# Optimization experiments

Measured on AMD Instinct MI355X. Metric: run time of the kernel, lower is better.

## Reference

```python
import jax, jax.numpy as jnp
import numpy as np

B = 8
H1c = W1c = 56
H2c = W2c = 112
C1 = 512
C2 = 256
NH = 8
WS = 7
POOL = 2
EPS = 1e-5


def setup_inputs() -> dict:
    key = jax.random.key(0)
    ks = jax.random.split(key, 8)
    x = jax.random.normal(ks[0], (B, H1c * W1c, C1), dtype=jnp.float32)
    y = jax.random.normal(ks[1], (B, H2c * W2c, C2), dtype=jnp.float32)
    Wq = jax.random.normal(ks[2], (C1, C1), dtype=jnp.float32) * 0.02
    Wkv = jax.random.normal(ks[3], (2 * C1, C2), dtype=jnp.float32) * 0.02
    Wproj = jax.random.normal(ks[4], (C1, C1), dtype=jnp.float32) * 0.02
    bproj = jnp.zeros((C1,), dtype=jnp.float32)
    # 1x1 conv: fan_out = out_channels -> std = sqrt(2/C2)
    Wsr = jax.random.normal(ks[5], (C2, C2), dtype=jnp.float32) * np.sqrt(2.0 / C2).astype(np.float32)
    bsr = jnp.zeros((C2,), dtype=jnp.float32)
    gn = jnp.ones((C2,), dtype=jnp.float32)
    bn = jnp.zeros((C2,), dtype=jnp.float32)
    return {"x": x, "y": y, "Wq": Wq, "Wkv": Wkv, "Wproj": Wproj,
            "bproj": bproj, "Wsr": Wsr, "bsr": bsr, "gn": gn, "bn": bn,
            "H1": H1c, "W1": W1c, "H2": H2c, "W2": W2c}


def _window_partition(t, ws):
    # t: (B, nh, H, W, C) -> (B*nh, num_windows, ws*ws, C)
    Bt, n, H, W, C = t.shape
    ht, wt = H // ws, W // ws
    t = t.reshape(Bt, n, ht, ws, wt, ws, C).transpose(0, 1, 2, 4, 3, 5, 6)
    return t.reshape(Bt * n, ht * wt, ws * ws, C)


def reference(x, y, Wq, Wkv, Wproj, bproj, Wsr, bsr, gn, bn, H1, W1, H2, W2):
    B1, N1, c1 = x.shape
    B2, N2, c2 = y.shape
    nh, ws = NH, WS
    hd = c1 // nh
    scale = hd ** (-0.5)

    # q projection -> (B, nh, H1, W1, hd)
    q = (x @ Wq.T).reshape(B1, H1, W1, nh, hd).transpose(0, 3, 1, 2, 4)

    # KV preprocessing: avgpool -> 1x1 conv -> layernorm -> gelu
    y2 = y.transpose(0, 2, 1).reshape(B2, c2, H2, W2)
    Hp, Wp = H2 // POOL, W2 // POOL
    y2 = y2.reshape(B2, c2, Hp, POOL, Wp, POOL).mean(axis=(3, 5))
    y2 = jnp.einsum('bchw,oc->bohw', y2, Wsr) + bsr[None, :, None, None]
    y2 = y2.reshape(B2, c2, Hp * Wp).transpose(0, 2, 1)  # (B, Np, C2)
    mu = y2.mean(-1, keepdims=True)
    var = y2.var(-1, keepdims=True)
    y2 = (y2 - mu) / jnp.sqrt(var + EPS) * gn + bn
    y2 = jax.nn.gelu(y2, approximate=False)

    kv = (y2 @ Wkv.T).reshape(B2, Hp * Wp, 2, nh, hd)
    k = kv[:, :, 0].transpose(0, 2, 1, 3).reshape(B2, nh, Hp, Wp, hd)
    v = kv[:, :, 1].transpose(0, 2, 1, 3).reshape(B2, nh, Hp, Wp, hd)

    qw = _window_partition(q, ws)   # (B*nh, nw, ws^2, hd)
    kw = _window_partition(k, ws)
    vw = _window_partition(v, ws)

    attn = jax.nn.softmax(jnp.einsum('bnqd,bnkd->bnqk', qw, kw) * scale, axis=-1)
    out = jnp.einsum('bnqk,bnkd->bnqd', attn, vw)  # (B*nh, nw, ws^2, hd)

    # window reverse -> (B, N1, C1)
    ht, wt = H1 // ws, W1 // ws
    out = out.reshape(B1, nh, ht, wt, ws, ws, hd).transpose(0, 1, 2, 4, 3, 5, 6)
    out = out.reshape(B1, nh, H1 * W1, hd).transpose(0, 2, 1, 3).reshape(B1, H1 * W1, c1)
    return out @ Wproj.T + bproj
```

## Files before the change

### kernel.cpp

```cpp
#include <hip/hip_runtime.h>
#include <hip/hip_bf16.h>

typedef __attribute__((ext_vector_type(8))) short short8;
typedef __attribute__((ext_vector_type(4))) float f32x4;
typedef __attribute__((ext_vector_type(4))) unsigned short ushort4v;

#define DI __device__ __forceinline__

DI unsigned short f2bf(float f) {
  union { float f; unsigned int u; } a; a.f = f;
  unsigned int u = a.u;
  return (unsigned short)((u + 0x7FFFu + ((u >> 16) & 1u)) >> 16);
}

#define BARRIER() do { asm volatile("" ::: "memory"); __builtin_amdgcn_s_barrier(); asm volatile("" ::: "memory"); } while (0)
#define GLOAD16(src, dst) __builtin_amdgcn_global_load_lds( \
    (const __attribute__((address_space(1))) void*)(src), \
    (__attribute__((address_space(3))) void*)(dst), 16, 0, 0)


__global__ __launch_bounds__(256)
void cvt_pool(const float* __restrict__ y, unsigned short* __restrict__ pooled,
              const float* __restrict__ Wq, const float* __restrict__ Wkv,
              const float* __restrict__ Wproj, const float* __restrict__ Wsr,
              unsigned short* __restrict__ Wq_b, unsigned short* __restrict__ Wkv_b,
              unsigned short* __restrict__ Wproj_b, unsigned short* __restrict__ Wsr_b) {
  int bid = blockIdx.x;
  if (bid < 6272) {
    int t = bid * 256 + threadIdx.x;
    int cv = (t & 63) * 4;
    int bp = t >> 6;
    int b = bp / 3136, p = bp % 3136;
    int hp = p / 56, wp = p % 56;
    const float* src = y + (((size_t)b * 12544) + hp * 224 + wp * 2) * 256 + cv;
    float4 a0 = *(const float4*)(src);
    float4 a1 = *(const float4*)(src + 256);
    float4 a2 = *(const float4*)(src + 28672);
    float4 a3 = *(const float4*)(src + 28672 + 256);
    float4 av;
    av.x = (a0.x + a1.x + a2.x + a3.x) * 0.25f;
    av.y = (a0.y + a1.y + a2.y + a3.y) * 0.25f;
    av.z = (a0.z + a1.z + a2.z + a3.z) * 0.25f;
    av.w = (a0.w + a1.w + a2.w + a3.w) * 0.25f;
    ushort4v o = { f2bf(av.x), f2bf(av.y), f2bf(av.z), f2bf(av.w) };
    *(ushort4v*)&pooled[(size_t)bp * 256 + cv] = o;
  } else {
    long i = (long)(bid - 6272) * 1024 + threadIdx.x * 4;
    const float* src; unsigned short* dst; long off;
    if (i < 262144L)      { src = Wq;    dst = Wq_b;    off = i; }
    else if (i < 524288L) { src = Wkv;   dst = Wkv_b;   off = i - 262144L; }
    else if (i < 786432L) { src = Wproj; dst = Wproj_b; off = i - 524288L; }
    else                  { src = Wsr;   dst = Wsr_b;   off = i - 786432L; }
    float4 v = *(const float4*)&src[off];
    ushort4v o = { f2bf(v.x), f2bf(v.y), f2bf(v.z), f2bf(v.w) };
    *(ushort4v*)&dst[off] = o;
  }
}

__global__ __launch_bounds__(256)
void sr_gemm(const unsigned short* __restrict__ Ap, const unsigned short* __restrict__ Wsr_b,
             const float* __restrict__ bsr, const float* __restrict__ gn,
             const float* __restrict__ bn, unsigned short* __restrict__ out) {
  __shared__ unsigned short sA[64 * 64];
  __shared__ unsigned short sB[256 * 64];
  __shared__ float red[64 * 8];

  const int tid = threadIdx.x;
  const int wv = tid >> 6;
  const int lane = tid & 63;
  const int lr = lane & 15;
  const int lg = lane >> 4;
  const int lr4 = lg * 4;
  const int m0 = blockIdx.x * 64;
  const int sr8 = lane >> 3;
  const int sl8 = lane & 7;

  f32x4 acc[4][4];
#pragma unroll
  for (int i = 0; i < 4; ++i)
#pragma unroll
    for (int j = 0; j < 4; ++j) acc[i][j] = (f32x4){0.f, 0.f, 0.f, 0.f};

  for (int kt = 0; kt < 256; kt += 64) {
#pragma unroll
    for (int c = 0; c < 2; ++c) {
      int row = wv * 16 + c * 8 + sr8;
      GLOAD16(Ap + (size_t)(m0 + row) * 256 + kt + ((sl8 ^ (row & 7)) * 8),
              &sA[(wv * 16 + c * 8) * 64]);
    }
#pragma unroll
    for (int c = 0; c < 8; ++c) {
      int row = wv * 64 + c * 8 + sr8;
      GLOAD16(Wsr_b + (size_t)row * 256 + kt + ((sl8 ^ (row & 7)) * 8),
              &sB[(wv * 64 + c * 8) * 64]);
    }
    __syncthreads();
#pragma unroll
    for (int ks = 0; ks < 2; ++ks) {
      short8 af[4], bfr[4];
#pragma unroll
      for (int i = 0; i < 4; ++i)
        af[i] = *(const short8*)&sA[(i * 16 + lr) * 64 + (((ks * 4 + lg) ^ (lr & 7)) * 8)];
#pragma unroll
      for (int j = 0; j < 4; ++j)
        bfr[j] = *(const short8*)&sB[(wv * 64 + j * 16 + lr) * 64 + (((ks * 4 + lg) ^ (lr & 7)) * 8)];
#pragma unroll
      for (int i = 0; i < 4; ++i)
#pragma unroll
        for (int j = 0; j < 4; ++j)
          acc[i][j] = __builtin_amdgcn_mfma_f32_16x16x32_bf16(af[i], bfr[j], acc[i][j], 0, 0, 0);
    }
    __syncthreads();
  }

  float bsv[4], gnv[4], bnv[4];
#pragma unroll
  for (int j = 0; j < 4; ++j) {
    int col = wv * 64 + j * 16 + lr;
    bsv[j] = bsr[col]; gnv[j] = gn[col]; bnv[j] = bn[col];
  }
  float s_[4][4], q_[4][4];
#pragma unroll
  for (int i = 0; i < 4; ++i)
#pragma unroll
    for (int r = 0; r < 4; ++r) {
      float s = 0.f, q = 0.f;
#pragma unroll
      for (int j = 0; j < 4; ++j) {
        float v = acc[i][j][r] + bsv[j];
        acc[i][j][r] = v;
        s += v; q += v * v;
      }
      s_[i][r] = s; q_[i][r] = q;
    }
#pragma unroll
  for (int m = 1; m <= 8; m <<= 1)
#pragma unroll
    for (int i = 0; i < 4; ++i)
#pragma unroll
      for (int r = 0; r < 4; ++r) {
        s_[i][r] += __shfl_xor(s_[i][r], m);
        q_[i][r] += __shfl_xor(q_[i][r], m);
      }
  if (lr == 0) {
#pragma unroll
    for (int i = 0; i < 4; ++i)
#pragma unroll
      for (int r = 0; r < 4; ++r) {
        int row = i * 16 + lr4 + r;
        red[row * 8 + wv * 2 + 0] = s_[i][r];
        red[row * 8 + wv * 2 + 1] = q_[i][r];
      }
  }
  __syncthreads();
#pragma unroll
  for (int i = 0; i < 4; ++i) {
#pragma unroll
    for (int r = 0; r < 4; ++r) {
      int row = i * 16 + lr4 + r;
      float sum = red[row * 8 + 0] + red[row * 8 + 2] + red[row * 8 + 4] + red[row * 8 + 6];
      float sq  = red[row * 8 + 1] + red[row * 8 + 3] + red[row * 8 + 5] + red[row * 8 + 7];
      float mean = sum * (1.f / 256.f);
      float var = sq * (1.f / 256.f) - mean * mean;
      float rstd = rsqrtf(var + 1e-5f);
#pragma unroll
      for (int j = 0; j < 4; ++j) {
        float t = (acc[i][j][r] - mean) * rstd * gnv[j] + bnv[j];
        t = 0.5f * t * (1.f + erff(t * 0.70710678118654752f));
        out[(size_t)(m0 + row) * 256 + wv * 64 + j * 16 + lr] = f2bf(t);
      }
    }
  }
}

DI void epi_q(int gm, int gc, float v, unsigned short* outp) {
  const int b = gm / 3136, pos = gm % 3136;
  const int h = pos / 56, ww = pos % 56;
  const int head = gc >> 6, d = gc & 63;
  const size_t idx = ((((size_t)(b * 8 + head)) * 64 + (h / 7) * 8 + (ww / 7)) * 49
                      + (h % 7) * 7 + (ww % 7)) * 64 + d;
  outp[idx] = f2bf(v);
}

template<int K, int N>
__global__ __launch_bounds__(512, 2)
void gemm256f(const float* __restrict__ A,
              const unsigned short* __restrict__ Bw,
              unsigned short* __restrict__ outp) {
  __shared__ unsigned short lds[65536];
  const int tid = threadIdx.x;
  const int wv = tid >> 6;
  const int lane = tid & 63;
  const int wm = wv >> 2;
  const int wn = wv & 3;
  const int m0 = blockIdx.y * 256;
  const int n0 = blockIdx.x * 256;
  const int lr = lane & 15;
  const int lg = lane >> 4;
  const int lr4 = lg * 4;
  const int srow8 = lane >> 3;
  const int sl8 = lane & 7;
  constexpr int NT = K / 64;

  f32x4 acc[8][4];
#pragma unroll
  for (int i = 0; i < 8; ++i)
#pragma unroll
    for (int j = 0; j < 4; ++j) acc[i][j] = (f32x4){0.f, 0.f, 0.f, 0.f};

  float4 fa[4][2];
  auto loadA = [&](int t1) {
    int tsrc = (t1 < NT) ? t1 : NT - 1;
#pragma unroll
    for (int rr = 0; rr < 4; ++rr) {
      int trow = rr * 64 + wv * 8 + srow8;
      const float* p = A + (size_t)(m0 + trow) * K + tsrc * 64 + sl8 * 8;
      fa[rr][0] = *(const float4*)p;
      fa[rr][1] = *(const float4*)(p + 4);
    }
    asm volatile("" ::: "memory");
  };
  auto writeA = [&](int t1) {
#pragma unroll
    for (int rr = 0; rr < 4; ++rr) {
      int trow = rr * 64 + wv * 8 + srow8;
      union { short8 s; unsigned short u[8]; } w;
      w.u[0] = f2bf(fa[rr][0].x); w.u[1] = f2bf(fa[rr][0].y);
      w.u[2] = f2bf(fa[rr][0].z); w.u[3] = f2bf(fa[rr][0].w);
      w.u[4] = f2bf(fa[rr][1].x); w.u[5] = f2bf(fa[rr][1].y);
      w.u[6] = f2bf(fa[rr][1].z); w.u[7] = f2bf(fa[rr][1].w);
      *(short8*)&lds[(t1 & 1) * 32768 + trow * 64 + ((sl8 ^ (trow & 7)) * 8)] = w.s;
    }
  };
  auto stageB = [&](int t1, int rr) {
    int tsrc = (t1 < NT) ? t1 : NT - 1;
    int trow = rr * 64 + wv * 8 + srow8;
    int sx = sl8 ^ (trow & 7);
    GLOAD16(Bw + (size_t)(n0 + trow) * K + tsrc * 64 + sx * 8,
            &lds[(t1 & 1) * 32768 + 16384 + (rr * 64 + wv * 8) * 64]);
  };
  auto rdA = [&](int s, int mf, int ks) -> short8 {
    int row = wm * 128 + mf * 16 + lr;
    int slot = ((ks << 2) + lg) ^ (row & 7);
    return *(const short8*)&lds[s * 32768 + row * 64 + slot * 8];
  };
  auto rdB = [&](int s, int nf, int ks) -> short8 {
    int row = wn * 64 + nf * 16 + lr;
    int slot = ((ks << 2) + lg) ^ (row & 7);
    return *(const short8*)&lds[s * 32768 + 16384 + row * 64 + slot * 8];
  };

  stageB(0, 0); stageB(0, 1); stageB(0, 2); stageB(0, 3);
  loadA(0);
  asm volatile("s_waitcnt vmcnt(0)" ::: "memory");
  writeA(0);
  asm volatile("s_waitcnt lgkmcnt(0)" ::: "memory");
  BARRIER();

  for (int t = 0; t < NT; ++t) {
    const int s = t & 1;
    short8 bfr[4][2];
    loadA(t + 1);
#pragma unroll
    for (int j = 0; j < 4; ++j) { bfr[j][0] = rdB(s, j, 0); bfr[j][1] = rdB(s, j, 1); }
    {
      short8 x0 = rdA(s, 0, 0), x1 = rdA(s, 0, 1);
      short8 y0 = rdA(s, 1, 0), y1 = rdA(s, 1, 1);
      BARRIER();
      __builtin_amdgcn_s_setprio(1);
#pragma unroll
      for (int j = 0; j < 4; ++j) {
        acc[0][j] = __builtin_amdgcn_mfma_f32_16x16x32_bf16(x0, bfr[j][0], acc[0][j], 0, 0, 0);
        acc[0][j] = __builtin_amdgcn_mfma_f32_16x16x32_bf16(x1, bfr[j][1], acc[0][j], 0, 0, 0);
        acc[1][j] = __builtin_amdgcn_mfma_f32_16x16x32_bf16(y0, bfr[j][0], acc[1][j], 0, 0, 0);
        acc[1][j] = __builtin_amdgcn_mfma_f32_16x16x32_bf16(y1, bfr[j][1], acc[1][j], 0, 0, 0);
      }
      __builtin_amdgcn_s_setprio(0);
      BARRIER();
    }
    stageB(t + 1, 0); stageB(t + 1, 1);
    {
      short8 x0 = rdA(s, 2, 0), x1 = rdA(s, 2, 1);
      short8 y0 = rdA(s, 3, 0), y1 = rdA(s, 3, 1);
      BARRIER();
      __builtin_amdgcn_s_setprio(1);
#pragma unroll
      for (int j = 0; j < 4; ++j) {
        acc[2][j] = __builtin_amdgcn_mfma_f32_16x16x32_bf16(x0, bfr[j][0], acc[2][j], 0, 0, 0);
        acc[2][j] = __builtin_amdgcn_mfma_f32_16x16x32_bf16(x1, bfr[j][1], acc[2][j], 0, 0, 0);
        acc[3][j] = __builtin_amdgcn_mfma_f32_16x16x32_bf16(y0, bfr[j][0], acc[3][j], 0, 0, 0);
        acc[3][j] = __builtin_amdgcn_mfma_f32_16x16x32_bf16(y1, bfr[j][1], acc[3][j], 0, 0, 0);
      }
      __builtin_amdgcn_s_setprio(0);
      BARRIER();
    }
    stageB(t + 1, 2); stageB(t + 1, 3);
    {
      short8 x0 = rdA(s, 4, 0), x1 = rdA(s, 4, 1);
      short8 y0 = rdA(s, 5, 0), y1 = rdA(s, 5, 1);
      BARRIER();
      __builtin_amdgcn_s_setprio(1);
#pragma unroll
      for (int j = 0; j < 4; ++j) {
        acc[4][j] = __builtin_amdgcn_mfma_f32_16x16x32_bf16(x0, bfr[j][0], acc[4][j], 0, 0, 0);
        acc[4][j] = __builtin_amdgcn_mfma_f32_16x16x32_bf16(x1, bfr[j][1], acc[4][j], 0, 0, 0);
        acc[5][j] = __builtin_amdgcn_mfma_f32_16x16x32_bf16(y0, bfr[j][0], acc[5][j], 0, 0, 0);
        acc[5][j] = __builtin_amdgcn_mfma_f32_16x16x32_bf16(y1, bfr[j][1], acc[5][j], 0, 0, 0);
      }
      __builtin_amdgcn_s_setprio(0);
      BARRIER();
    }
    {
      short8 x0 = rdA(s, 6, 0), x1 = rdA(s, 6, 1);
      short8 y0 = rdA(s, 7, 0), y1 = rdA(s, 7, 1);
      asm volatile("s_waitcnt vmcnt(4)" ::: "memory");
      writeA(t + 1);
      asm volatile("s_waitcnt lgkmcnt(0)" ::: "memory");
      BARRIER();
      __builtin_amdgcn_s_setprio(1);
#pragma unroll
      for (int j = 0; j < 4; ++j) {
        acc[6][j] = __builtin_amdgcn_mfma_f32_16x16x32_bf16(x0, bfr[j][0], acc[6][j], 0, 0, 0);
        acc[6][j] = __builtin_amdgcn_mfma_f32_16x16x32_bf16(x1, bfr[j][1], acc[6][j], 0, 0, 0);
        acc[7][j] = __builtin_amdgcn_mfma_f32_16x16x32_bf16(y0, bfr[j][0], acc[7][j], 0, 0, 0);
        acc[7][j] = __builtin_amdgcn_mfma_f32_16x16x32_bf16(y1, bfr[j][1], acc[7][j], 0, 0, 0);
      }
      __builtin_amdgcn_s_setprio(0);
      asm volatile("s_waitcnt vmcnt(0)" ::: "memory");
      BARRIER();
    }
  }

#pragma unroll
  for (int i = 0; i < 8; ++i)
#pragma unroll
    for (int j = 0; j < 4; ++j)
#pragma unroll
      for (int r = 0; r < 4; ++r)
        epi_q(m0 + wm * 128 + i * 16 + lr4 + r, n0 + wn * 64 + j * 16 + lr,
              acc[i][j][r], outp);
}

__global__ __launch_bounds__(1024)
void kvattn(const unsigned short* __restrict__ y2,
            const unsigned short* __restrict__ Wkv_b,
            const unsigned short* __restrict__ qwin,
            const unsigned short* __restrict__ Wproj_b,
            const float* __restrict__ bproj,
            float* __restrict__ out) {
  __shared__ unsigned short lds[81920];
  const int tid = threadIdx.x;
  const int wv16 = tid >> 6;
  const int head = wv16 >> 1;
  const int half = wv16 & 1;
  const int lane = tid & 63;
  const int lr = lane & 15;
  const int lg = lane >> 4;
  const int r8 = lane >> 3;
  const int sl8 = lane & 7;
  const int bb = blockIdx.x >> 6;
  const int win = blockIdx.x & 63;
  const int ht = win >> 3, wt = win & 7;

  unsigned short* Cy  = lds;
  unsigned short* SLh = lds + 16384 + head * 8192;
  unsigned short* OA  = lds + 16384;
  unsigned short* WPs = lds + 49152 + wv16 * 2048;

  {
    int rb = wv16 & 7;
    int m = rb * 8 + r8;
    int mm = (m < 49) ? m : 48;
    int grow = bb * 3136 + (ht * 7 + mm / 7) * 56 + wt * 7 + (mm % 7);
    int p0 = wv16 >> 3;
#pragma unroll
    for (int pp = 0; pp < 2; ++pp) {
      int panel = p0 + pp * 2;
      GLOAD16(y2 + (size_t)grow * 256 + panel * 64 + ((sl8 ^ (m & 7)) * 8),
              &Cy[panel * 4096 + rb * 512]);
    }
  }

  auto stageW = [&](int s) {
    int h2 = s >> 2, kt = s & 3;
#pragma unroll
    for (int c = 0; c < 4; ++c) {
      int lrow = half * 32 + c * 8 + r8;
      GLOAD16(Wkv_b + (size_t)(h2 * 512 + head * 64 + lrow) * 256 + kt * 64 + ((sl8 ^ r8) * 8),
              &SLh[(s & 1) * 4096 + (half * 32 + c * 8) * 64]);
    }
  };

  f32x4 aK[4][2], aV[4][2];
#pragma unroll
  for (int i = 0; i < 4; ++i)
#pragma unroll
    for (int j = 0; j < 2; ++j) { aK[i][j] = (f32x4){0,0,0,0}; aV[i][j] = (f32x4){0,0,0,0}; }

  stageW(0);
  asm volatile("s_waitcnt vmcnt(4)" ::: "memory");
  BARRIER();

#pragma unroll
  for (int s = 0; s < 8; ++s) {
    if (s < 7) {
      stageW(s + 1);
      asm volatile("s_waitcnt vmcnt(4)" ::: "memory");
    } else {
      asm volatile("s_waitcnt vmcnt(0)" ::: "memory");
    }
    const int kt = s & 3;
    const unsigned short* Wb = &SLh[(s & 1) * 4096];
    short8 bfrg[2][2];
#pragma unroll
    for (int nf2 = 0; nf2 < 2; ++nf2)
#pragma unroll
      for (int ks = 0; ks < 2; ++ks) {
        int row = (half * 2 + nf2) * 16 + lr;
        bfrg[nf2][ks] = *(const short8*)&Wb[row * 64 + (((ks * 4 + lg) ^ (lr & 7)) * 8)];
      }
#pragma unroll
    for (int mf = 0; mf < 4; ++mf)
#pragma unroll
      for (int ks = 0; ks < 2; ++ks) {
        short8 af = *(const short8*)&Cy[kt * 4096 + (mf * 16 + lr) * 64 + (((ks * 4 + lg) ^ (lr & 7)) * 8)];
#pragma unroll
        for (int nf2 = 0; nf2 < 2; ++nf2) {
          if (s < 4)
            aK[mf][nf2] = __builtin_amdgcn_mfma_f32_16x16x32_bf16(af, bfrg[nf2][ks], aK[mf][nf2], 0, 0, 0);
          else
            aV[mf][nf2] = __builtin_amdgcn_mfma_f32_16x16x32_bf16(af, bfrg[nf2][ks], aV[mf][nf2], 0, 0, 0);
        }
      }
  }

  const unsigned short* qb = qwin + (size_t)((bb * 8 + head) * 64 + win) * 3136;
  short8 qf[2][2];
#pragma unroll
  for (int mf2 = 0; mf2 < 2; ++mf2)
#pragma unroll
    for (int ks = 0; ks < 2; ++ks)
      qf[mf2][ks] = *(const short8*)&qb[((half * 2 + mf2) * 16 + lr) * 64 + ks * 32 + lg * 8];

  BARRIER();

#pragma unroll
  for (int mf = 0; mf < 4; ++mf)
#pragma unroll
    for (int nf2 = 0; nf2 < 2; ++nf2)
#pragma unroll
      for (int r = 0; r < 4; ++r) {
        int key = mf * 16 + lg * 4 + r;
        int d = (half * 2 + nf2) * 16 + lr;
        SLh[key * 64 + (((d >> 3) ^ (key & 7)) * 8) + (d & 7)] = f2bf(aK[mf][nf2][r]);
        SLh[4096 + d * 64 + (((key >> 3) ^ (d & 7)) * 8) + (key & 7)] = f2bf(aV[mf][nf2][r]);
      }
  asm volatile("s_waitcnt lgkmcnt(0)" ::: "memory");
  BARRIER();

  f32x4 aS[2][4];
#pragma unroll
  for (int i = 0; i < 2; ++i)
#pragma unroll
    for (int j = 0; j < 4; ++j) aS[i][j] = (f32x4){0,0,0,0};
#pragma unroll
  for (int mf2 = 0; mf2 < 2; ++mf2)
#pragma unroll
    for (int ks = 0; ks < 2; ++ks)
#pragma unroll
      for (int nf = 0; nf < 4; ++nf) {
        short8 bk = *(const short8*)&SLh[(nf * 16 + lr) * 64 + (((ks * 4 + lg) ^ (lr & 7)) * 8)];
        aS[mf2][nf] = __builtin_amdgcn_mfma_f32_16x16x32_bf16(qf[mf2][ks], bk, aS[mf2][nf], 0, 0, 0);
      }

#pragma unroll
  for (int nf = 0; nf < 4; ++nf)
    if (nf * 16 + lr >= 49) {
#pragma unroll
      for (int mf2 = 0; mf2 < 2; ++mf2)
#pragma unroll
        for (int r = 0; r < 4; ++r) aS[mf2][nf][r] = -1e30f;
    }
  const float cexp = 0.125f * 1.4426950408889634f;
  float mx[2][4], sm[2][4];
#pragma unroll
  for (int mf2 = 0; mf2 < 2; ++mf2)
#pragma unroll
    for (int r = 0; r < 4; ++r)
      mx[mf2][r] = fmaxf(fmaxf(aS[mf2][0][r], aS[mf2][1][r]), fmaxf(aS[mf2][2][r], aS[mf2][3][r]));
#pragma unroll
  for (int m = 1; m <= 8; m <<= 1)
#pragma unroll
    for (int mf2 = 0; mf2 < 2; ++mf2)
#pragma unroll
      for (int r = 0; r < 4; ++r) mx[mf2][r] = fmaxf(mx[mf2][r], __shfl_xor(mx[mf2][r], m));
#pragma unroll
  for (int mf2 = 0; mf2 < 2; ++mf2)
#pragma unroll
    for (int nf = 0; nf < 4; ++nf)
#pragma unroll
      for (int r = 0; r < 4; ++r)
        aS[mf2][nf][r] = exp2f((aS[mf2][nf][r] - mx[mf2][r]) * cexp);
#pragma unroll
  for (int mf2 = 0; mf2 < 2; ++mf2)
#pragma unroll
    for (int r = 0; r < 4; ++r)
      sm[mf2][r] = aS[mf2][0][r] + aS[mf2][1][r] + aS[mf2][2][r] + aS[mf2][3][r];
#pragma unroll
  for (int m = 1; m <= 8; m <<= 1)
#pragma unroll
    for (int mf2 = 0; mf2 < 2; ++mf2)
#pragma unroll
      for (int r = 0; r < 4; ++r) sm[mf2][r] += __shfl_xor(sm[mf2][r], m);
#pragma unroll
  for (int mf2 = 0; mf2 < 2; ++mf2)
#pragma unroll
    for (int r = 0; r < 4; ++r) sm[mf2][r] = 1.f / sm[mf2][r];

  BARRIER();

#pragma unroll
  for (int mf2 = 0; mf2 < 2; ++mf2)
#pragma unroll
    for (int nf = 0; nf < 4; ++nf)
#pragma unroll
      for (int r = 0; r < 4; ++r) {
        int q = (half * 2 + mf2) * 16 + lg * 4 + r;
        int key = nf * 16 + lr;
        SLh[q * 64 + (((key >> 3) ^ (q & 7)) * 8) + (key & 7)] = f2bf(aS[mf2][nf][r] * sm[mf2][r]);
      }

  f32x4 aO[2][4];
#pragma unroll
  for (int i = 0; i < 2; ++i)
#pragma unroll
    for (int j = 0; j < 4; ++j) aO[i][j] = (f32x4){0,0,0,0};
#pragma unroll
  for (int mf2 = 0; mf2 < 2; ++mf2)
#pragma unroll
    for (int ks = 0; ks < 2; ++ks) {
      int qrow = (half * 2 + mf2) * 16 + lr;
      short8 pf = *(const short8*)&SLh[qrow * 64 + (((ks * 4 + lg) ^ (lr & 7)) * 8)];
#pragma unroll
      for (int df = 0; df < 4; ++df) {
        short8 vf = *(const short8*)&SLh[4096 + (df * 16 + lr) * 64 + (((ks * 4 + lg) ^ (lr & 7)) * 8)];
        aO[mf2][df] = __builtin_amdgcn_mfma_f32_16x16x32_bf16(pf, vf, aO[mf2][df], 0, 0, 0);
      }
    }

  BARRIER();

#pragma unroll
  for (int mf2 = 0; mf2 < 2; ++mf2)
#pragma unroll
    for (int df = 0; df < 4; ++df)
#pragma unroll
      for (int r = 0; r < 4; ++r) {
        int q = (half * 2 + mf2) * 16 + lg * 4 + r;
        int slot = df * 2 + (lr >> 3);
        OA[q * 512 + head * 64 + ((slot ^ (q & 7)) * 8) + (lr & 7)] = f2bf(aO[mf2][df][r]);
      }
#pragma unroll
  for (int c = 0; c < 4; ++c) {
    int lrow = c * 8 + r8;
    GLOAD16(Wproj_b + (size_t)(head * 64 + half * 32 + lrow) * 512 + ((sl8 ^ r8) * 8),
            &WPs[c * 512]);
  }
  asm volatile("s_waitcnt lgkmcnt(0) vmcnt(0)" ::: "memory");
  BARRIER();

  f32x4 aR[4][2];
#pragma unroll
  for (int i = 0; i < 4; ++i)
#pragma unroll
    for (int j = 0; j < 2; ++j) aR[i][j] = (f32x4){0,0,0,0};
#pragma unroll
  for (int kt = 0; kt < 8; ++kt) {
    short8 nx[4];
    if (kt < 7) {
#pragma unroll
      for (int c = 0; c < 4; ++c) {
        int lrow = c * 8 + r8;
        nx[c] = *(const short8*)&Wproj_b[(size_t)(head * 64 + half * 32 + lrow) * 512
                                         + (kt + 1) * 64 + ((sl8 ^ r8) * 8)];
      }
    }
#pragma unroll
    for (int mf = 0; mf < 4; ++mf)
#pragma unroll
      for (int ks = 0; ks < 2; ++ks) {
        short8 af2 = *(const short8*)&OA[(mf * 16 + lr) * 512 + kt * 64 + (((ks * 4 + lg) ^ (lr & 7)) * 8)];
#pragma unroll
        for (int nf2 = 0; nf2 < 2; ++nf2) {
          short8 bf2 = *(const short8*)&WPs[(nf2 * 16 + lr) * 64 + (((ks * 4 + lg) ^ (lr & 7)) * 8)];
          aR[mf][nf2] = __builtin_amdgcn_mfma_f32_16x16x32_bf16(af2, bf2, aR[mf][nf2], 0, 0, 0);
        }
      }
    if (kt < 7) {
#pragma unroll
      for (int c = 0; c < 4; ++c)
        *(short8*)&WPs[(c * 8 + r8) * 64 + sl8 * 8] = nx[c];
    }
  }

#pragma unroll
  for (int mf = 0; mf < 4; ++mf)
#pragma unroll
    for (int nf2 = 0; nf2 < 2; ++nf2)
#pragma unroll
      for (int r = 0; r < 4; ++r) {
        int q = mf * 16 + lg * 4 + r;
        if (q < 49) {
          int gm = bb * 3136 + (ht * 7 + q / 7) * 56 + wt * 7 + (q % 7);
          int col = head * 64 + (half * 2 + nf2) * 16 + lr;
          out[(size_t)gm * 512 + col] = aR[mf][nf2][r] + bproj[col];
        }
      }
}

extern "C" void kernel_launch(void* const* d_in, const int* in_sizes, int n_in,
                              void* d_out, int out_size, void* d_ws, size_t ws_size,
                              hipStream_t stream) {
  const float* x     = (const float*)d_in[0];
  const float* y     = (const float*)d_in[1];
  const float* Wq    = (const float*)d_in[2];
  const float* Wkv   = (const float*)d_in[3];
  const float* Wproj = (const float*)d_in[4];
  const float* bproj = (const float*)d_in[5];
  const float* Wsr   = (const float*)d_in[6];
  const float* bsr   = (const float*)d_in[7];
  const float* gn    = (const float*)d_in[8];
  const float* bn    = (const float*)d_in[9];
  float* out = (float*)d_out;

  char* ws = (char*)d_ws;
  unsigned short* Wq_b    = (unsigned short*)ws; ws += 524288;
  unsigned short* Wkv_b   = (unsigned short*)ws; ws += 524288;
  unsigned short* Wproj_b = (unsigned short*)ws; ws += 524288;
  unsigned short* Wsr_b   = (unsigned short*)ws; ws += 131072;
  unsigned short* regA    = (unsigned short*)ws; ws += 12845056;
  unsigned short* q_win   = (unsigned short*)ws; ws += 25690112;
  unsigned short* regC    = (unsigned short*)ws; ws += 12845056;

  cvt_pool<<<7104, 256, 0, stream>>>(y, regA, Wq, Wkv, Wproj, Wsr,
                                     Wq_b, Wkv_b, Wproj_b, Wsr_b);

  gemm256f<512, 512><<<dim3(2, 98), 512, 0, stream>>>(x, Wq_b, q_win);

  sr_gemm<<<392, 256, 0, stream>>>(regA, Wsr_b, bsr, gn, bn, regC);

  kvattn<<<512, 1024, 0, stream>>>(regC, Wkv_b, q_win, Wproj_b, bproj, out);
}
```

Baseline: 139.8 us.

## Merge Q projection and SR conv GEMMs into one launch; vectorize V LDS stores

Combines the Q-projection GEMM and the spatial-reduction GEMM+LayerNorm+GELU into a single kernel launch with 392 blocks. The first 196 blocks run the Q GEMM and the remaining 196 run the SR GEMM, now on 128-row tiles with 512 threads. The aim is to remove one launch and let the two independent GEMMs share the GPU at the same time, since the Q GEMM alone underfills it. Separately, the V transpose store into LDS in kvattn is packed into 4-element vector writes. The risk is that the SR blocks inherit the larger LDS allocation and the launch bounds sized for the Q GEMM, which may lower occupancy.

```diff
diff --git a/kernel.cpp b/kernel.cpp
--- a/kernel.cpp
+++ b/kernel.cpp
@@ -57,122 +57,6 @@
   }
 }
 
-__global__ __launch_bounds__(256)
-void sr_gemm(const unsigned short* __restrict__ Ap, const unsigned short* __restrict__ Wsr_b,
-             const float* __restrict__ bsr, const float* __restrict__ gn,
-             const float* __restrict__ bn, unsigned short* __restrict__ out) {
-  __shared__ unsigned short sA[64 * 64];
-  __shared__ unsigned short sB[256 * 64];
-  __shared__ float red[64 * 8];
-
-  const int tid = threadIdx.x;
-  const int wv = tid >> 6;
-  const int lane = tid & 63;
-  const int lr = lane & 15;
-  const int lg = lane >> 4;
-  const int lr4 = lg * 4;
-  const int m0 = blockIdx.x * 64;
-  const int sr8 = lane >> 3;
-  const int sl8 = lane & 7;
-
-  f32x4 acc[4][4];
-#pragma unroll
-  for (int i = 0; i < 4; ++i)
-#pragma unroll
-    for (int j = 0; j < 4; ++j) acc[i][j] = (f32x4){0.f, 0.f, 0.f, 0.f};
-
-  for (int kt = 0; kt < 256; kt += 64) {
-#pragma unroll
-    for (int c = 0; c < 2; ++c) {
-      int row = wv * 16 + c * 8 + sr8;
-      GLOAD16(Ap + (size_t)(m0 + row) * 256 + kt + ((sl8 ^ (row & 7)) * 8),
-              &sA[(wv * 16 + c * 8) * 64]);
-    }
-#pragma unroll
-    for (int c = 0; c < 8; ++c) {
-      int row = wv * 64 + c * 8 + sr8;
-      GLOAD16(Wsr_b + (size_t)row * 256 + kt + ((sl8 ^ (row & 7)) * 8),
-              &sB[(wv * 64 + c * 8) * 64]);
-    }
-    __syncthreads();
-#pragma unroll
-    for (int ks = 0; ks < 2; ++ks) {
-      short8 af[4], bfr[4];
-#pragma unroll
-      for (int i = 0; i < 4; ++i)
-        af[i] = *(const short8*)&sA[(i * 16 + lr) * 64 + (((ks * 4 + lg) ^ (lr & 7)) * 8)];
-#pragma unroll
-      for (int j = 0; j < 4; ++j)
-        bfr[j] = *(const short8*)&sB[(wv * 64 + j * 16 + lr) * 64 + (((ks * 4 + lg) ^ (lr & 7)) * 8)];
-#pragma unroll
-      for (int i = 0; i < 4; ++i)
-#pragma unroll
-        for (int j = 0; j < 4; ++j)
-          acc[i][j] = __builtin_amdgcn_mfma_f32_16x16x32_bf16(af[i], bfr[j], acc[i][j], 0, 0, 0);
-    }
-    __syncthreads();
-  }
-
-  float bsv[4], gnv[4], bnv[4];
-#pragma unroll
-  for (int j = 0; j < 4; ++j) {
-    int col = wv * 64 + j * 16 + lr;
-    bsv[j] = bsr[col]; gnv[j] = gn[col]; bnv[j] = bn[col];
-  }
-  float s_[4][4], q_[4][4];
-#pragma unroll
-  for (int i = 0; i < 4; ++i)
-#pragma unroll
-    for (int r = 0; r < 4; ++r) {
-      float s = 0.f, q = 0.f;
-#pragma unroll
-      for (int j = 0; j < 4; ++j) {
-        float v = acc[i][j][r] + bsv[j];
-        acc[i][j][r] = v;
-        s += v; q += v * v;
-      }
-      s_[i][r] = s; q_[i][r] = q;
-    }
-#pragma unroll
-  for (int m = 1; m <= 8; m <<= 1)
-#pragma unroll
-    for (int i = 0; i < 4; ++i)
-#pragma unroll
-      for (int r = 0; r < 4; ++r) {
-        s_[i][r] += __shfl_xor(s_[i][r], m);
-        q_[i][r] += __shfl_xor(q_[i][r], m);
-      }
-  if (lr == 0) {
-#pragma unroll
-    for (int i = 0; i < 4; ++i)
-#pragma unroll
-      for (int r = 0; r < 4; ++r) {
-        int row = i * 16 + lr4 + r;
-        red[row * 8 + wv * 2 + 0] = s_[i][r];
-        red[row * 8 + wv * 2 + 1] = q_[i][r];
-      }
-  }
-  __syncthreads();
-#pragma unroll
-  for (int i = 0; i < 4; ++i) {
-#pragma unroll
-    for (int r = 0; r < 4; ++r) {
-      int row = i * 16 + lr4 + r;
-      float sum = red[row * 8 + 0] + red[row * 8 + 2] + red[row * 8 + 4] + red[row * 8 + 6];
-      float sq  = red[row * 8 + 1] + red[row * 8 + 3] + red[row * 8 + 5] + red[row * 8 + 7];
-      float mean = sum * (1.f / 256.f);
-      float var = sq * (1.f / 256.f) - mean * mean;
-      float rstd = rsqrtf(var + 1e-5f);
-#pragma unroll
-      for (int j = 0; j < 4; ++j) {
-        float t = (acc[i][j][r] - mean) * rstd * gnv[j] + bnv[j];
-        t = 0.5f * t * (1.f + erff(t * 0.70710678118654752f));
-        out[(size_t)(m0 + row) * 256 + wv * 64 + j * 16 + lr] = f2bf(t);
-      }
-    }
-  }
-}
-
 DI void epi_q(int gm, int gc, float v, unsigned short* outp) {
   const int b = gm / 3136, pos = gm % 3136;
   const int h = pos / 56, ww = pos % 56;
@@ -182,163 +66,275 @@
   outp[idx] = f2bf(v);
 }
 
-template<int K, int N>
 __global__ __launch_bounds__(512, 2)
-void gemm256f(const float* __restrict__ A,
+void qsr_gemm(const float* __restrict__ A,
               const unsigned short* __restrict__ Bw,
-              unsigned short* __restrict__ outp) {
+              unsigned short* __restrict__ outp,
+              const unsigned short* __restrict__ Ap,
+              const unsigned short* __restrict__ Wsr_b,
+              const float* __restrict__ bsr, const float* __restrict__ gn,
+              const float* __restrict__ bn, unsigned short* __restrict__ y2out) {
   __shared__ unsigned short lds[65536];
+  const int bid = blockIdx.x;
   const int tid = threadIdx.x;
   const int wv = tid >> 6;
   const int lane = tid & 63;
-  const int wm = wv >> 2;
-  const int wn = wv & 3;
-  const int m0 = blockIdx.y * 256;
-  const int n0 = blockIdx.x * 256;
   const int lr = lane & 15;
   const int lg = lane >> 4;
   const int lr4 = lg * 4;
   const int srow8 = lane >> 3;
   const int sl8 = lane & 7;
-  constexpr int NT = K / 64;
-
-  f32x4 acc[8][4];
-#pragma unroll
-  for (int i = 0; i < 8; ++i)
-#pragma unroll
-    for (int j = 0; j < 4; ++j) acc[i][j] = (f32x4){0.f, 0.f, 0.f, 0.f};
-
-  float4 fa[4][2];
-  auto loadA = [&](int t1) {
-    int tsrc = (t1 < NT) ? t1 : NT - 1;
-#pragma unroll
-    for (int rr = 0; rr < 4; ++rr) {
+
+  if (bid < 196) {
+    const int wm = wv >> 2;
+    const int wn = wv & 3;
+    const int m0 = (bid >> 1) * 256;
+    const int n0 = (bid & 1) * 256;
+    constexpr int K = 512, NT = K / 64;
+
+    f32x4 acc[8][4];
+#pragma unroll
+    for (int i = 0; i < 8; ++i)
+#pragma unroll
+      for (int j = 0; j < 4; ++j) acc[i][j] = (f32x4){0.f, 0.f, 0.f, 0.f};
+
+    float4 fa[4][2];
+    auto loadA = [&](int t1) {
+      int tsrc = (t1 < NT) ? t1 : NT - 1;
+#pragma unroll
+      for (int rr = 0; rr < 4; ++rr) {
+        int trow = rr * 64 + wv * 8 + srow8;
+        const float* p = A + (size_t)(m0 + trow) * K + tsrc * 64 + sl8 * 8;
+        fa[rr][0] = *(const float4*)p;
+        fa[rr][1] = *(const float4*)(p + 4);
+      }
+      asm volatile("" ::: "memory");
+    };
+    auto writeA = [&](int t1) {
+#pragma unroll
+      for (int rr = 0; rr < 4; ++rr) {
+        int trow = rr * 64 + wv * 8 + srow8;
+        union { short8 s; unsigned short u[8]; } w;
+        w.u[0] = f2bf(fa[rr][0].x); w.u[1] = f2bf(fa[rr][0].y);
+        w.u[2] = f2bf(fa[rr][0].z); w.u[3] = f2bf(fa[rr][0].w);
+        w.u[4] = f2bf(fa[rr][1].x); w.u[5] = f2bf(fa[rr][1].y);
+        w.u[6] = f2bf(fa[rr][1].z); w.u[7] = f2bf(fa[rr][1].w);
+        *(short8*)&lds[(t1 & 1) * 32768 + trow * 64 + ((sl8 ^ (trow & 7)) * 8)] = w.s;
+      }
+    };
+    auto stageB = [&](int t1, int rr) {
+      int tsrc = (t1 < NT) ? t1 : NT - 1;
       int trow = rr * 64 + wv * 8 + srow8;
-      const float* p = A + (size_t)(m0 + trow) * K + tsrc * 64 + sl8 * 8;
-      fa[rr][0] = *(const float4*)p;
-      fa[rr][1] = *(const float4*)(p + 4);
-    }
-    asm volatile("" ::: "memory");
-  };
-  auto writeA = [&](int t1) {
-#pragma unroll
-    for (int rr = 0; rr < 4; ++rr) {
-      int trow = rr * 64 + wv * 8 + srow8;
-      union { short8 s; unsigned short u[8]; } w;
-      w.u[0] = f2bf(fa[rr][0].x); w.u[1] = f2bf(fa[rr][0].y);
-      w.u[2] = f2bf(fa[rr][0].z); w.u[3] = f2bf(fa[rr][0].w);
-      w.u[4] = f2bf(fa[rr][1].x); w.u[5] = f2bf(fa[rr][1].y);
-      w.u[6] = f2bf(fa[rr][1].z); w.u[7] = f2bf(fa[rr][1].w);
-      *(short8*)&lds[(t1 & 1) * 32768 + trow * 64 + ((sl8 ^ (trow & 7)) * 8)] = w.s;
-    }
-  };
-  auto stageB = [&](int t1, int rr) {
-    int tsrc = (t1 < NT) ? t1 : NT - 1;
-    int trow = rr * 64 + wv * 8 + srow8;
-    int sx = sl8 ^ (trow & 7);
-    GLOAD16(Bw + (size_t)(n0 + trow) * K + tsrc * 64 + sx * 8,
-            &lds[(t1 & 1) * 32768 + 16384 + (rr * 64 + wv * 8) * 64]);
-  };
-  auto rdA = [&](int s, int mf, int ks) -> short8 {
-    int row = wm * 128 + mf * 16 + lr;
-    int slot = ((ks << 2) + lg) ^ (row & 7);
-    return *(const short8*)&lds[s * 32768 + row * 64 + slot * 8];
-  };
-  auto rdB = [&](int s, int nf, int ks) -> short8 {
-    int row = wn * 64 + nf * 16 + lr;
-    int slot = ((ks << 2) + lg) ^ (row & 7);
-    return *(const short8*)&lds[s * 32768 + 16384 + row * 64 + slot * 8];
-  };
-
-  stageB(0, 0); stageB(0, 1); stageB(0, 2); stageB(0, 3);
-  loadA(0);
-  asm volatile("s_waitcnt vmcnt(0)" ::: "memory");
-  writeA(0);
-  asm volatile("s_waitcnt lgkmcnt(0)" ::: "memory");
-  BARRIER();
-
-  for (int t = 0; t < NT; ++t) {
-    const int s = t & 1;
-    short8 bfr[4][2];
-    loadA(t + 1);
-#pragma unroll
-    for (int j = 0; j < 4; ++j) { bfr[j][0] = rdB(s, j, 0); bfr[j][1] = rdB(s, j, 1); }
-    {
-      short8 x0 = rdA(s, 0, 0), x1 = rdA(s, 0, 1);
-      short8 y0 = rdA(s, 1, 0), y1 = rdA(s, 1, 1);
-      BARRIER();
-      __builtin_amdgcn_s_setprio(1);
-#pragma unroll
-      for (int j = 0; j < 4; ++j) {
-        acc[0][j] = __builtin_amdgcn_mfma_f32_16x16x32_bf16(x0, bfr[j][0], acc[0][j], 0, 0, 0);
-        acc[0][j] = __builtin_amdgcn_mfma_f32_16x16x32_bf16(x1, bfr[j][1], acc[0][j], 0, 0, 0);
-        acc[1][j] = __builtin_amdgcn_mfma_f32_16x16x32_bf16(y0, bfr[j][0], acc[1][j], 0, 0, 0);
-        acc[1][j] = __builtin_amdgcn_mfma_f32_16x16x32_bf16(y1, bfr[j][1], acc[1][j], 0, 0, 0);
-      }
-      __builtin_amdgcn_s_setprio(0);
-      BARRIER();
-    }
-    stageB(t + 1, 0); stageB(t + 1, 1);
-    {
-      short8 x0 = rdA(s, 2, 0), x1 = rdA(s, 2, 1);
-      short8 y0 = rdA(s, 3, 0), y1 = rdA(s, 3, 1);
-      BARRIER();
-      __builtin_amdgcn_s_setprio(1);
-#pragma unroll
-      for (int j = 0; j < 4; ++j) {
-        acc[2][j] = __builtin_amdgcn_mfma_f32_16x16x32_bf16(x0, bfr[j][0], acc[2][j], 0, 0, 0);
-        acc[2][j] = __builtin_amdgcn_mfma_f32_16x16x32_bf16(x1, bfr[j][1], acc[2][j], 0, 0, 0);
-        acc[3][j] = __builtin_amdgcn_mfma_f32_16x16x32_bf16(y0, bfr[j][0], acc[3][j], 0, 0, 0);
-        acc[3][j] = __builtin_amdgcn_mfma_f32_16x16x32_bf16(y1, bfr[j][1], acc[3][j], 0, 0, 0);
-      }
-      __builtin_amdgcn_s_setprio(0);
-      BARRIER();
-    }
-    stageB(t + 1, 2); stageB(t + 1, 3);
-    {
-      short8 x0 = rdA(s, 4, 0), x1 = rdA(s, 4, 1);
-      short8 y0 = rdA(s, 5, 0), y1 = rdA(s, 5, 1);
-      BARRIER();
-      __builtin_amdgcn_s_setprio(1);
-#pragma unroll
-      for (int j = 0; j < 4; ++j) {
-        acc[4][j] = __builtin_amdgcn_mfma_f32_16x16x32_bf16(x0, bfr[j][0], acc[4][j], 0, 0, 0);
-        acc[4][j] = __builtin_amdgcn_mfma_f32_16x16x32_bf16(x1, bfr[j][1], acc[4][j], 0, 0, 0);
-        acc[5][j] = __builtin_amdgcn_mfma_f32_16x16x32_bf16(y0, bfr[j][0], acc[5][j], 0, 0, 0);
-        acc[5][j] = __builtin_amdgcn_mfma_f32_16x16x32_bf16(y1, bfr[j][1], acc[5][j], 0, 0, 0);
-      }
-      __builtin_amdgcn_s_setprio(0);
-      BARRIER();
-    }
-    {
-      short8 x0 = rdA(s, 6, 0), x1 = rdA(s, 6, 1);
-      short8 y0 = rdA(s, 7, 0), y1 = rdA(s, 7, 1);
-      asm volatile("s_waitcnt vmcnt(4)" ::: "memory");
-      writeA(t + 1);
-      asm volatile("s_waitcnt lgkmcnt(0)" ::: "memory");
-      BARRIER();
-      __builtin_amdgcn_s_setprio(1);
-#pragma unroll
-      for (int j = 0; j < 4; ++j) {
-        acc[6][j] = __builtin_amdgcn_mfma_f32_16x16x32_bf16(x0, bfr[j][0], acc[6][j], 0, 0, 0);
-        acc[6][j] = __builtin_amdgcn_mfma_f32_16x16x32_bf16(x1, bfr[j][1], acc[6][j], 0, 0, 0);
-        acc[7][j] = __builtin_amdgcn_mfma_f32_16x16x32_bf16(y0, bfr[j][0], acc[7][j], 0, 0, 0);
-        acc[7][j] = __builtin_amdgcn_mfma_f32_16x16x32_bf16(y1, bfr[j][1], acc[7][j], 0, 0, 0);
-      }
-      __builtin_amdgcn_s_setprio(0);
-      asm volatile("s_waitcnt vmcnt(0)" ::: "memory");
-      BARRIER();
+      int sx = sl8 ^ (trow & 7);
+      GLOAD16(Bw + (size_t)(n0 + trow) * K + tsrc * 64 + sx * 8,
+              &lds[(t1 & 1) * 32768 + 16384 + (rr * 64 + wv * 8) * 64]);
+    };
+    auto rdA = [&](int s, int mf, int ks) -> short8 {
+      int row = wm * 128 + mf * 16 + lr;
+      int slot = ((ks << 2) + lg) ^ (row & 7);
+      return *(const short8*)&lds[s * 32768 + row * 64 + slot * 8];
+    };
+    auto rdB = [&](int s, int nf, int ks) -> short8 {
+      int row = wn * 64 + nf * 16 + lr;
+      int slot = ((ks << 2) + lg) ^ (row & 7);
+      return *(const short8*)&lds[s * 32768 + 16384 + row * 64 + slot * 8];
+    };
+
+    stageB(0, 0); stageB(0, 1); stageB(0, 2); stageB(0, 3);
+    loadA(0);
+    asm volatile("s_waitcnt vmcnt(0)" ::: "memory");
+    writeA(0);
+    asm volatile("s_waitcnt lgkmcnt(0)" ::: "memory");
+    BARRIER();
+
+    for (int t = 0; t < NT; ++t) {
+      const int s = t & 1;
+      short8 bfr[4][2];
+      loadA(t + 1);
+#pragma unroll
+      for (int j = 0; j < 4; ++j) { bfr[j][0] = rdB(s, j, 0); bfr[j][1] = rdB(s, j, 1); }
+      {
+        short8 x0 = rdA(s, 0, 0), x1 = rdA(s, 0, 1);
+        short8 y0 = rdA(s, 1, 0), y1 = rdA(s, 1, 1);
+        BARRIER();
+        __builtin_amdgcn_s_setprio(1);
+#pragma unroll
+        for (int j = 0; j < 4; ++j) {
+          acc[0][j] = __builtin_amdgcn_mfma_f32_16x16x32_bf16(x0, bfr[j][0], acc[0][j], 0, 0, 0);
+          acc[0][j] = __builtin_amdgcn_mfma_f32_16x16x32_bf16(x1, bfr[j][1], acc[0][j], 0, 0, 0);
+          acc[1][j] = __builtin_amdgcn_mfma_f32_16x16x32_bf16(y0, bfr[j][0], acc[1][j], 0, 0, 0);
+          acc[1][j] = __builtin_amdgcn_mfma_f32_16x16x32_bf16(y1, bfr[j][1], acc[1][j], 0, 0, 0);
+        }
+        __builtin_amdgcn_s_setprio(0);
+        BARRIER();
+      }
+      stageB(t + 1, 0); stageB(t + 1, 1);
+      {
+        short8 x0 = rdA(s, 2, 0), x1 = rdA(s, 2, 1);
+        short8 y0 = rdA(s, 3, 0), y1 = rdA(s, 3, 1);
+        BARRIER();
+        __builtin_amdgcn_s_setprio(1);
+#pragma unroll
+        for (int j = 0; j < 4; ++j) {
+          acc[2][j] = __builtin_amdgcn_mfma_f32_16x16x32_bf16(x0, bfr[j][0], acc[2][j], 0, 0, 0);
+          acc[2][j] = __builtin_amdgcn_mfma_f32_16x16x32_bf16(x1, bfr[j][1], acc[2][j], 0, 0, 0);
+          acc[3][j] = __builtin_amdgcn_mfma_f32_16x16x32_bf16(y0, bfr[j][0], acc[3][j], 0, 0, 0);
+          acc[3][j] = __builtin_amdgcn_mfma_f32_16x16x32_bf16(y1, bfr[j][1], acc[3][j], 0, 0, 0);
+        }
+        __builtin_amdgcn_s_setprio(0);
+        BARRIER();
+      }
+      stageB(t + 1, 2); stageB(t + 1, 3);
+      {
+        short8 x0 = rdA(s, 4, 0), x1 = rdA(s, 4, 1);
+        short8 y0 = rdA(s, 5, 0), y1 = rdA(s, 5, 1);
+        BARRIER();
+        __builtin_amdgcn_s_setprio(1);
+#pragma unroll
+        for (int j = 0; j < 4; ++j) {
+          acc[4][j] = __builtin_amdgcn_mfma_f32_16x16x32_bf16(x0, bfr[j][0], acc[4][j], 0, 0, 0);
+          acc[4][j] = __builtin_amdgcn_mfma_f32_16x16x32_bf16(x1, bfr[j][1], acc[4][j], 0, 0, 0);
+          acc[5][j] = __builtin_amdgcn_mfma_f32_16x16x32_bf16(y0, bfr[j][0], acc[5][j], 0, 0, 0);
+          acc[5][j] = __builtin_amdgcn_mfma_f32_16x16x32_bf16(y1, bfr[j][1], acc[5][j], 0, 0, 0);
+        }
+        __builtin_amdgcn_s_setprio(0);
+        BARRIER();
+      }
+      {
+        short8 x0 = rdA(s, 6, 0), x1 = rdA(s, 6, 1);
+        short8 y0 = rdA(s, 7, 0), y1 = rdA(s, 7, 1);
+        asm volatile("s_waitcnt vmcnt(4)" ::: "memory");
+        writeA(t + 1);
+        asm volatile("s_waitcnt lgkmcnt(0)" ::: "memory");
+        BARRIER();
+        __builtin_amdgcn_s_setprio(1);
+#pragma unroll
+        for (int j = 0; j < 4; ++j) {
+          acc[6][j] = __builtin_amdgcn_mfma_f32_16x16x32_bf16(x0, bfr[j][0], acc[6][j], 0, 0, 0);
+          acc[6][j] = __builtin_amdgcn_mfma_f32_16x16x32_bf16(x1, bfr[j][1], acc[6][j], 0, 0, 0);
+          acc[7][j] = __builtin_amdgcn_mfma_f32_16x16x32_bf16(y0, bfr[j][0], acc[7][j], 0, 0, 0);
+          acc[7][j] = __builtin_amdgcn_mfma_f32_16x16x32_bf16(y1, bfr[j][1], acc[7][j], 0, 0, 0);
+        }
+        __builtin_amdgcn_s_setprio(0);
+        asm volatile("s_waitcnt vmcnt(0)" ::: "memory");
+        BARRIER();
+      }
+    }
+
+#pragma unroll
+    for (int i = 0; i < 8; ++i)
+#pragma unroll
+      for (int j = 0; j < 4; ++j)
+#pragma unroll
+        for (int r = 0; r < 4; ++r)
+          epi_q(m0 + wm * 128 + i * 16 + lr4 + r, n0 + wn * 64 + j * 16 + lr,
+                acc[i][j][r], outp);
+  } else {
+    unsigned short* sA = lds;
+    unsigned short* sB = lds + 8192;
+    float* red = (float*)&lds[24576];
+    const int tl = wv >> 2;
+    const int w4 = wv & 3;
+    const int m0 = (bid - 196) * 128;
+
+    f32x4 acc[4][4];
+#pragma unroll
+    for (int i = 0; i < 4; ++i)
+#pragma unroll
+      for (int j = 0; j < 4; ++j) acc[i][j] = (f32x4){0.f, 0.f, 0.f, 0.f};
+
+    for (int kt = 0; kt < 256; kt += 64) {
+#pragma unroll
+      for (int c = 0; c < 2; ++c) {
+        int row = tl * 64 + w4 * 16 + c * 8 + srow8;
+        GLOAD16(Ap + (size_t)(m0 + row) * 256 + kt + ((sl8 ^ srow8) * 8),
+                &sA[row * 64]);
+      }
+#pragma unroll
+      for (int c = 0; c < 4; ++c) {
+        int row = wv * 32 + c * 8 + srow8;
+        GLOAD16(Wsr_b + (size_t)row * 256 + kt + ((sl8 ^ srow8) * 8),
+                &sB[row * 64]);
+      }
+      __syncthreads();
+#pragma unroll
+      for (int ks = 0; ks < 2; ++ks) {
+        short8 af[4], bfr[4];
+#pragma unroll
+        for (int i = 0; i < 4; ++i)
+          af[i] = *(const short8*)&sA[(tl * 64 + i * 16 + lr) * 64 + (((ks * 4 + lg) ^ (lr & 7)) * 8)];
+#pragma unroll
+        for (int j = 0; j < 4; ++j)
+          bfr[j] = *(const short8*)&sB[(w4 * 64 + j * 16 + lr) * 64 + (((ks * 4 + lg) ^ (lr & 7)) * 8)];
+#pragma unroll
+        for (int i = 0; i < 4; ++i)
+#pragma unroll
+          for (int j = 0; j < 4; ++j)
+            acc[i][j] = __builtin_amdgcn_mfma_f32_16x16x32_bf16(af[i], bfr[j], acc[i][j], 0, 0, 0);
+      }
+      __syncthreads();
+    }
+
+    float bsv[4], gnv[4], bnv[4];
+#pragma unroll
+    for (int j = 0; j < 4; ++j) {
+      int col = w4 * 64 + j * 16 + lr;
+      bsv[j] = bsr[col]; gnv[j] = gn[col]; bnv[j] = bn[col];
+    }
+    float s_[4][4], q_[4][4];
+#pragma unroll
+    for (int i = 0; i < 4; ++i)
+#pragma unroll
+      for (int r = 0; r < 4; ++r) {
+        float s = 0.f, q = 0.f;
+#pragma unroll
+        for (int j = 0; j < 4; ++j) {
+          float v = acc[i][j][r] + bsv[j];
+          acc[i][j][r] = v;
+          s += v; q += v * v;
+        }
+        s_[i][r] = s; q_[i][r] = q;
+      }
+#pragma unroll
+    for (int m = 1; m <= 8; m <<= 1)
+#pragma unroll
+      for (int i = 0; i < 4; ++i)
+#pragma unroll
+        for (int r = 0; r < 4; ++r) {
+          s_[i][r] += __shfl_xor(s_[i][r], m);
+          q_[i][r] += __shfl_xor(q_[i][r], m);
+        }
+    if (lr == 0) {
+#pragma unroll
+      for (int i = 0; i < 4; ++i)
+#pragma unroll
+        for (int r = 0; r < 4; ++r) {
+          int row = i * 16 + lr4 + r;
+          red[(tl * 64 + row) * 8 + w4 * 2 + 0] = s_[i][r];
+          red[(tl * 64 + row) * 8 + w4 * 2 + 1] = q_[i][r];
+        }
+    }
+    __syncthreads();
+#pragma unroll
+    for (int i = 0; i < 4; ++i) {
+#pragma unroll
+      for (int r = 0; r < 4; ++r) {
+        int row = i * 16 + lr4 + r;
+        const float* rd = &red[(tl * 64 + row) * 8];
+        float sum = rd[0] + rd[2] + rd[4] + rd[6];
+        float sq  = rd[1] + rd[3] + rd[5] + rd[7];
+        float mean = sum * (1.f / 256.f);
+        float var = sq * (1.f / 256.f) - mean * mean;
+        float rstd = rsqrtf(var + 1e-5f);
+#pragma unroll
+        for (int j = 0; j < 4; ++j) {
+          float t = (acc[i][j][r] - mean) * rstd * gnv[j] + bnv[j];
+          t = 0.5f * t * (1.f + erff(t * 0.70710678118654752f));
+          y2out[(size_t)(m0 + tl * 64 + row) * 256 + w4 * 64 + j * 16 + lr] = f2bf(t);
+        }
+      }
     }
   }
-
-#pragma unroll
-  for (int i = 0; i < 8; ++i)
-#pragma unroll
-    for (int j = 0; j < 4; ++j)
-#pragma unroll
-      for (int r = 0; r < 4; ++r)
-        epi_q(m0 + wm * 128 + i * 16 + lr4 + r, n0 + wn * 64 + j * 16 + lr,
-              acc[i][j][r], outp);
 }
 
 __global__ __launch_bounds__(1024)
@@ -447,14 +443,18 @@
 #pragma unroll
   for (int mf = 0; mf < 4; ++mf)
 #pragma unroll
-    for (int nf2 = 0; nf2 < 2; ++nf2)
+    for (int nf2 = 0; nf2 < 2; ++nf2) {
+      int d = (half * 2 + nf2) * 16 + lr;
 #pragma unroll
       for (int r = 0; r < 4; ++r) {
         int key = mf * 16 + lg * 4 + r;
-        int d = (half * 2 + nf2) * 16 + lr;
         SLh[key * 64 + (((d >> 3) ^ (key & 7)) * 8) + (d & 7)] = f2bf(aK[mf][nf2][r]);
-        SLh[4096 + d * 64 + (((key >> 3) ^ (d & 7)) * 8) + (key & 7)] = f2bf(aV[mf][nf2][r]);
-      }
+      }
+      int slotv = (mf * 2 + (lg >> 1)) ^ (d & 7);
+      ushort4v pv = { f2bf(aV[mf][nf2][0]), f2bf(aV[mf][nf2][1]),
+                      f2bf(aV[mf][nf2][2]), f2bf(aV[mf][nf2][3]) };
+      *(ushort4v*)&SLh[4096 + d * 64 + slotv * 8 + (lg & 1) * 4] = pv;
+    }
   asm volatile("s_waitcnt lgkmcnt(0)" ::: "memory");
   BARRIER();
 
@@ -645,9 +645,8 @@
   cvt_pool<<<7104, 256, 0, stream>>>(y, regA, Wq, Wkv, Wproj, Wsr,
                                      Wq_b, Wkv_b, Wproj_b, Wsr_b);
 
-  gemm256f<512, 512><<<dim3(2, 98), 512, 0, stream>>>(x, Wq_b, q_win);
-
-  sr_gemm<<<392, 256, 0, stream>>>(regA, Wsr_b, bsr, gn, bn, regC);
+  qsr_gemm<<<392, 512, 0, stream>>>(x, Wq_b, q_win,
+                                    regA, Wsr_b, bsr, gn, bn, regC);
 
   kvattn<<<512, 1024, 0, stream>>>(regC, Wkv_b, q_win, Wproj_b, bproj, out);
 }
```

Result: no change. 138.0 us, median of 2 (-1.3%).
